# Kernel optimization log

Measured on AMD Instinct MI355X. Metric: run time of the kernel, lower is better.

Reference implementation:

```python
import jax, jax.numpy as jnp
import numpy as np

# dims: NL layers, D=d_model, DI=expand*D, F=d_ff, V=vocab, L=S*C seq, R=dt_rank, N=d_state, K=d_conv
NL, D, DI, F, V, L, R, N, K = 2, 256, 512, 1024, 1024, 1024, 16, 16, 4
B, S, C = 2, 128, 8
EPS = 1e-5


def silu(x):
    return x * jax.nn.sigmoid(x)


def batchnorm(x, g, b):  # x: [B,L,D], normalize over (B,L) per channel (training-mode BatchNorm1d)
    m = x.mean((0, 1))
    v = x.var((0, 1))
    return (x - m) * jax.lax.rsqrt(v + EPS) * g + b


def layernorm(x, g, b):
    m = x.mean(-1, keepdims=True)
    v = x.var(-1, keepdims=True)
    return (x - m) * jax.lax.rsqrt(v + EPS) * g + b


def mamba(x, Win, cw, cb, Wx, Wdt, bdt, A_log, Dsk, Wout, bout):
    # x: [B,L,D] -> [B,L,D]; standard Mamba block with selective scan
    Bsz, Lseq, _ = x.shape
    xz = x @ Win                      # [B,L,2*DI]
    xi, z = jnp.split(xz, 2, axis=-1)
    # depthwise causal conv1d, width K
    xp = jnp.pad(xi, ((0, 0), (K - 1, 0), (0, 0)))
    xc = cb + sum(xp[:, k:k + Lseq, :] * cw[:, k] for k in range(K))
    xc = silu(xc)                     # [B,L,DI]
    xdb = xc @ Wx                     # [B,L,R+2N]
    delta = jax.nn.softplus(xdb[..., :R] @ Wdt + bdt)   # [B,L,DI]
    Bm = xdb[..., R:R + N]            # [B,L,N]
    Cm = xdb[..., R + N:]             # [B,L,N]
    A = -jnp.exp(A_log)               # [DI,N]
    dA = jnp.exp(delta[..., None] * A)                       # [B,L,DI,N]
    dBx = delta[..., None] * Bm[:, :, None, :] * xc[..., None]  # [B,L,DI,N]

    def step(h, inp):
        dA_t, dBx_t, C_t = inp
        h = h * dA_t + dBx_t          # [B,DI,N]
        y = jnp.einsum('bdn,bn->bd', h, C_t)
        return h, y

    h0 = jnp.zeros((Bsz, DI, N), x.dtype)
    _, ys = jax.lax.scan(step, h0, (dA.transpose(1, 0, 2, 3), dBx.transpose(1, 0, 2, 3), Cm.transpose(1, 0, 2)))
    y = ys.transpose(1, 0, 2) + Dsk * xc
    y = y * silu(z)
    return y @ Wout + bout


def _forward(input_ids, emb, pos, Win, conv_w, conv_b, Wx, Wdt, bdt, A_log, Dskip, Wout, bout,
             bn_g, bn_b, ln_g, ln_b, ff_w1, ff_b1, ff_w2, ff_b2, final_w, final_b):
    Bsz, Ssz, Csz = input_ids.shape
    Lseq = Ssz * Csz
    # Encoder: token embedding (scaled) + learned positions, flattened to [B, S*C, D]
    x = emb[input_ids].reshape(Bsz, Lseq, D) * jnp.sqrt(jnp.float32(D)) + pos[:Lseq]
    for i in range(NL):
        f = mamba(x, Win[i, 0], conv_w[i, 0], conv_b[i, 0], Wx[i, 0], Wdt[i, 0], bdt[i, 0],
                  A_log[i, 0], Dskip[i, 0], Wout[i, 0], bout[i, 0])
        f = batchnorm(f, bn_g[i, 0], bn_b[i, 0])
        bk = mamba(x[:, ::-1], Win[i, 1], conv_w[i, 1], conv_b[i, 1], Wx[i, 1], Wdt[i, 1], bdt[i, 1],
                   A_log[i, 1], Dskip[i, 1], Wout[i, 1], bout[i, 1])
        bk = batchnorm(bk, bn_g[i, 1], bn_b[i, 1])[:, ::-1]
        f = layernorm(x + f, ln_g[i, 0], ln_b[i, 0])
        bk = layernorm(x + bk, ln_g[i, 1], ln_b[i, 1])
        out = f + bk
        out = jax.nn.relu(out @ ff_w1[i] + ff_b1[i]) @ ff_w2[i] + ff_b2[i]
        out = batchnorm(out, bn_g[i, 2], bn_b[i, 2])
        x = out + x
    return x.reshape(Bsz, Ssz, Csz, D) @ final_w + final_b   # [B,S,C,V]


def setup_inputs() -> dict:
    key = jax.random.key(0)
    ks = list(jax.random.split(key, 16))
    kit = iter(ks)
    rn = lambda shape, s=0.02: jax.random.normal(next(kit), shape, jnp.float32) * s
    inp = {
        'input_ids': jax.random.randint(next(kit), (B, S, C), 0, V),
        'emb': rn((V, D)), 'pos': rn((L, D)),
        'Win': rn((NL, 2, D, 2 * DI)),
        'conv_w': rn((NL, 2, DI, K), 0.1), 'conv_b': jnp.zeros((NL, 2, DI)),
        'Wx': rn((NL, 2, DI, R + 2 * N)),
        'Wdt': rn((NL, 2, R, DI)), 'bdt': jnp.full((NL, 2, DI), -4.0),
        'A_log': jnp.broadcast_to(jnp.log(jnp.arange(1, N + 1, dtype=jnp.float32)), (NL, 2, DI, N)) + 0.0,
        'Dskip': jnp.ones((NL, 2, DI)),
        'Wout': rn((NL, 2, DI, D)), 'bout': jnp.zeros((NL, 2, D)),
        'bn_g': jnp.ones((NL, 3, D)), 'bn_b': jnp.zeros((NL, 3, D)),
        'ln_g': jnp.ones((NL, 2, D)), 'ln_b': jnp.zeros((NL, 2, D)),
        'ff_w1': rn((NL, D, F)), 'ff_b1': jnp.zeros((NL, F)),
        'ff_w2': rn((NL, F, D)), 'ff_b2': jnp.zeros((NL, D)),
        'final_w': rn((D, V)), 'final_b': jnp.zeros((V,)),
    }
    return inp


def reference(input_ids, emb, pos, Win, conv_w, conv_b, Wx, Wdt, bdt, A_log, Dskip, Wout, bout,
              bn_g, bn_b, ln_g, ln_b, ff_w1, ff_b1, ff_w2, ff_b2, final_w, final_b):
    return _forward(input_ids, emb, pos, Win, conv_w, conv_b, Wx, Wdt, bdt, A_log, Dskip, Wout, bout,
                    bn_g, bn_b, ln_g, ln_b, ff_w1, ff_b1, ff_w2, ff_b2, final_w, final_b)
```

## Files before the change

kernel.cpp:

```cpp
#include <hip/hip_runtime.h>

#define NL 2
#define DMODEL 256
#define DI 512
#define FF 1024
#define VV 1024
#define LSEQ 1024
#define RR 16
#define NN 16
#define KCONV 4
#define BTOK 2048
#define EPS 1e-5f

using short8 = __attribute__((ext_vector_type(8))) short;
using float4v = __attribute__((ext_vector_type(4))) float;
typedef unsigned short u16;

__device__ inline float bf2f(u16 u) {
    union { unsigned u; float f; } x; x.u = (unsigned)u << 16; return x.f;
}
__device__ inline u16 f2bf(float f) {
    union { float f; unsigned u; } x; x.f = f;
    unsigned r = x.u + 0x7fffu + ((x.u >> 16) & 1u);
    return (u16)(r >> 16);
}

#if __has_builtin(__builtin_amdgcn_exp2f)
#define EXP2(x) __builtin_amdgcn_exp2f(x)
#else
#define EXP2(x) exp2f(x)
#endif

struct TMat { const float* src; u16* dst; int rows, cols, tile0, tilecols; };
struct TTable { TMat m[24]; int nmat; };

__global__ __launch_bounds__(256) void transpose_kernel(TTable tt) {
    __shared__ u16 tile[32][33];
    int bx = blockIdx.x;
    int j = 0;
    for (int k = 1; k < tt.nmat; ++k) if (bx >= tt.m[k].tile0) j = k;
    TMat mm = tt.m[j];
    int lt = bx - mm.tile0;
    int r0 = (lt / mm.tilecols) * 32, c0 = (lt % mm.tilecols) * 32;
    int tx = threadIdx.x & 31, ty = threadIdx.x >> 5;
    #pragma unroll
    for (int k = 0; k < 4; ++k) {
        int r = r0 + ty + k * 8, c = c0 + tx;
        tile[ty + k * 8][tx] = (r < mm.rows && c < mm.cols) ? f2bf(mm.src[(size_t)r * mm.cols + c]) : (u16)0;
    }
    __syncthreads();
    #pragma unroll
    for (int k = 0; k < 4; ++k) {
        int c = c0 + ty + k * 8, r = r0 + tx;
        if (c < mm.cols && r < mm.rows) mm.dst[(size_t)c * mm.rows + r] = tile[tx][ty + k * 8];
    }
}

template<int BN, int WR, int WC, int RT, int CT>
__global__ __launch_bounds__(256) void sgemm_kernel(
    const u16* __restrict__ A0, int lda, unsigned long long sA,
    const u16* __restrict__ B0, int ldb, unsigned long long sB,
    const float* __restrict__ bias0, unsigned long long sBias,
    void* __restrict__ C0, int ldc, unsigned long long sC,
    int K, int act, int outfp)
{
    constexpr int BM = 128, BK = 32;
    __shared__ u16 As[BM * BK];
    __shared__ u16 Bs[BN * BK];
    const u16* A = A0 + (size_t)blockIdx.z * sA;
    const u16* Bt = B0 + (size_t)blockIdx.z * sB;
    const float* bias = bias0 ? (bias0 + (size_t)blockIdx.z * sBias) : nullptr;

    const int tid = threadIdx.x, w = tid >> 6, lane = tid & 63;
    const int row0 = blockIdx.y * BM, col0 = blockIdx.x * BN;
    const int wr = w / WC, wc = w % WC;
    const int mi = lane & 15, kq = lane >> 4;
    const int lr = lane >> 2, lc = (lane & 3) * 8;

    float4v acc[RT][CT];
    #pragma unroll
    for (int i = 0; i < RT; ++i)
        #pragma unroll
        for (int j = 0; j < CT; ++j) acc[i][j] = (float4v){0.f, 0.f, 0.f, 0.f};

    for (int kk = 0; kk < K; kk += BK) {
        __syncthreads();
        for (int i = w; i < BM / 16; i += 4) {
            const u16* g = A + (size_t)(row0 + i * 16 + lr) * lda + kk + lc;
            __builtin_amdgcn_global_load_lds(
                (const __attribute__((address_space(1))) void*)g,
                (__attribute__((address_space(3))) void*)(As + i * 16 * BK), 16, 0, 0);
        }
        for (int i = w; i < BN / 16; i += 4) {
            const u16* g = Bt + (size_t)(col0 + i * 16 + lr) * ldb + kk + lc;
            __builtin_amdgcn_global_load_lds(
                (const __attribute__((address_space(1))) void*)g,
                (__attribute__((address_space(3))) void*)(Bs + i * 16 * BK), 16, 0, 0);
        }
        __syncthreads();
        short8 af[RT], bf[CT];
        #pragma unroll
        for (int i = 0; i < RT; ++i)
            af[i] = *(const short8*)(As + (wr * RT * 16 + i * 16 + mi) * BK + kq * 8);
        #pragma unroll
        for (int j = 0; j < CT; ++j)
            bf[j] = *(const short8*)(Bs + (wc * CT * 16 + j * 16 + mi) * BK + kq * 8);
        #pragma unroll
        for (int i = 0; i < RT; ++i)
            #pragma unroll
            for (int j = 0; j < CT; ++j)
                acc[i][j] = __builtin_amdgcn_mfma_f32_16x16x32_bf16(af[i], bf[j], acc[i][j], 0, 0, 0);
    }

    #pragma unroll
    for (int i = 0; i < RT; ++i)
        #pragma unroll
        for (int j = 0; j < CT; ++j) {
            int n = col0 + wc * CT * 16 + j * 16 + mi;
            float bv = bias ? bias[n] : 0.f;
            #pragma unroll
            for (int r = 0; r < 4; ++r) {
                int m = row0 + wr * RT * 16 + i * 16 + kq * 4 + r;
                float v = acc[i][j][r] + bv;
                if (act == 1) v = fmaxf(v, 0.f);
                if (outfp)
                    ((float*)C0)[(size_t)blockIdx.z * sC + (size_t)m * ldc + n] = v;
                else
                    ((u16*)C0)[(size_t)blockIdx.z * sC + (size_t)m * ldc + n] = f2bf(v);
            }
        }
}

__global__ __launch_bounds__(256) void gemm_kernel(
    const u16* __restrict__ A0, int lda, unsigned long long sA,
    const u16* __restrict__ B0, int ldb, unsigned long long sB,
    const float* __restrict__ bias0, unsigned long long sBias,
    void* __restrict__ C0, int ldc, unsigned long long sC,
    int M, int N, int K, int act, int outfp)
{
    const u16* A = A0 + (size_t)blockIdx.z * sA;
    const u16* Bt = B0 + (size_t)blockIdx.z * sB;
    const float* bias = bias0 ? (bias0 + (size_t)blockIdx.z * sBias) : nullptr;

    int tid = threadIdx.x;
    int wv = tid >> 6, lane = tid & 63;
    int row0 = blockIdx.y * 64 + (wv >> 1) * 32;
    int col0 = blockIdx.x * 64 + (wv & 1) * 32;
    int mi = lane & 15, kq = lane >> 4;

    float4v acc[2][2];
    #pragma unroll
    for (int a = 0; a < 2; ++a)
        #pragma unroll
        for (int b = 0; b < 2; ++b) acc[a][b] = (float4v){0.f, 0.f, 0.f, 0.f};
    const short8 zer = {0, 0, 0, 0, 0, 0, 0, 0};

    for (int kk = 0; kk < K; kk += 32) {
        int k = kk + kq * 8;
        bool kv = (k < K);
        short8 af[2], bf[2];
        #pragma unroll
        for (int rt = 0; rt < 2; ++rt) {
            int r = row0 + rt * 16 + mi;
            af[rt] = kv ? *(const short8*)(A + (size_t)r * lda + k) : zer;
        }
        #pragma unroll
        for (int ct = 0; ct < 2; ++ct) {
            int n = col0 + ct * 16 + mi;
            bf[ct] = (kv && n < N) ? *(const short8*)(Bt + (size_t)n * ldb + k) : zer;
        }
        #pragma unroll
        for (int rt = 0; rt < 2; ++rt)
            #pragma unroll
            for (int ct = 0; ct < 2; ++ct)
                acc[rt][ct] = __builtin_amdgcn_mfma_f32_16x16x32_bf16(af[rt], bf[ct], acc[rt][ct], 0, 0, 0);
    }

    #pragma unroll
    for (int rt = 0; rt < 2; ++rt)
        #pragma unroll
        for (int ct = 0; ct < 2; ++ct) {
            int n = col0 + ct * 16 + mi;
            if (n >= N) continue;
            float bv = bias ? bias[n] : 0.f;
            #pragma unroll
            for (int r = 0; r < 4; ++r) {
                int m = row0 + rt * 16 + kq * 4 + r;
                float v = acc[rt][ct][r] + bv;
                if (act == 1) v = fmaxf(v, 0.f);
                if (outfp)
                    ((float*)C0)[(size_t)blockIdx.z * sC + (size_t)m * ldc + n] = v;
                else
                    ((u16*)C0)[(size_t)blockIdx.z * sC + (size_t)m * ldc + n] = f2bf(v);
            }
        }
}

__global__ __launch_bounds__(256) void delta_fused_kernel(
    const u16* __restrict__ xdb, const u16* __restrict__ wdtT,
    const float* __restrict__ bdt, const u16* __restrict__ xc,
    u16* __restrict__ deltaT, u16* __restrict__ uT, int layer)
{
    int z = blockIdx.z;
    const u16* A = xdb + (size_t)z * BTOK * 48;
    const u16* Bt = wdtT + (size_t)z * 512 * 16;
    const float* bias = bdt + (size_t)z * 512;

    int tid = threadIdx.x;
    int wv = tid >> 6, lane = tid & 63;
    int row0 = blockIdx.y * 64 + (wv >> 1) * 32;
    int col0 = blockIdx.x * 64 + (wv & 1) * 32;
    int mi = lane & 15, kq = lane >> 4;

    float4v acc[2][2];
    #pragma unroll
    for (int a = 0; a < 2; ++a)
        #pragma unroll
        for (int b = 0; b < 2; ++b) acc[a][b] = (float4v){0.f, 0.f, 0.f, 0.f};
    const short8 zer = {0, 0, 0, 0, 0, 0, 0, 0};

    int k = kq * 8;
    bool kv = (k < 16);
    short8 af[2], bf[2];
    #pragma unroll
    for (int rt = 0; rt < 2; ++rt) {
        int r = row0 + rt * 16 + mi;
        af[rt] = kv ? *(const short8*)(A + (size_t)r * 48 + k) : zer;
    }
    #pragma unroll
    for (int ct = 0; ct < 2; ++ct) {
        int n = col0 + ct * 16 + mi;
        bf[ct] = kv ? *(const short8*)(Bt + (size_t)n * 16 + k) : zer;
    }
    #pragma unroll
    for (int rt = 0; rt < 2; ++rt)
        #pragma unroll
        for (int ct = 0; ct < 2; ++ct)
            acc[rt][ct] = __builtin_amdgcn_mfma_f32_16x16x32_bf16(af[rt], bf[ct], acc[rt][ct], 0, 0, 0);

    #pragma unroll
    for (int rt = 0; rt < 2; ++rt)
        #pragma unroll
        for (int ct = 0; ct < 2; ++ct) {
            int n = col0 + ct * 16 + mi;
            float bv = bias[n];
            #pragma unroll
            for (int r = 0; r < 4; ++r) {
                int m = row0 + rt * 16 + kq * 4 + r;
                float v = acc[rt][ct][r] + bv;
                v = (v > 20.f) ? v : logf(1.f + __expf(v));
                float xcv = bf2f(xc[((size_t)z * BTOK + m) * DI + n]);
                int b = m >> 10, t = m & 1023;
                size_t off = ((size_t)((z * 2 + b) * DI + n)) * LSEQ + t;
                deltaT[off] = f2bf(v);
                uT[off] = f2bf(v * xcv);
            }
        }
}

__global__ __launch_bounds__(256) void bct_kernel(
    const u16* __restrict__ xdb, u16* __restrict__ bcT)
{
    __shared__ u16 tile[32][34];
    int slab = blockIdx.y;
    int t0 = blockIdx.x * 32;
    int tx = threadIdx.x & 31, ty = threadIdx.x >> 5;
    #pragma unroll
    for (int k = 0; k < 4; ++k) {
        int t = t0 + ty + k * 8;
        tile[tx][ty + k * 8] = xdb[(size_t)(slab * 1024 + t) * 48 + 16 + tx];
    }
    __syncthreads();
    #pragma unroll
    for (int k = 0; k < 4; ++k) {
        int col = ty + k * 8;
        bcT[((size_t)(slab * 32 + col)) * LSEQ + t0 + tx] = tile[col][tx];
    }
}

__global__ __launch_bounds__(256) void embed_kernel(
    const int* __restrict__ ids, const float* __restrict__ emb,
    const float* __restrict__ pos, u16* __restrict__ x)
{
    int tok = blockIdx.x, d = threadIdx.x;
    int id = ids[tok];
    float v = emb[(size_t)id * DMODEL + d] * 16.0f + pos[(size_t)(tok & (LSEQ - 1)) * DMODEL + d];
    x[(size_t)tok * DMODEL + d] = f2bf(v);
}

__global__ __launch_bounds__(256) void conv_kernel(
    const u16* __restrict__ xz, const float* __restrict__ conv_w,
    const float* __restrict__ conv_b, u16* __restrict__ xc, int layer)
{
    unsigned g = blockIdx.x * 256u + threadIdx.x;
    int d = g & 511;
    int t = (g >> 9) & 1023;
    int b = (g >> 19) & 1;
    int dir = g >> 20;
    int wbase = ((layer * 2 + dir) * DI + d);
    float acc = conv_b[wbase];
    int colbase = dir * 1024 + d;
    #pragma unroll
    for (int k = 0; k < KCONV; ++k) {
        int ts = dir ? (t + 3 - k) : (t - 3 + k);
        if (ts >= 0 && ts < LSEQ)
            acc += conv_w[wbase * KCONV + k] * bf2f(xz[(size_t)((b << 10) + ts) * 2048 + colbase]);
    }
    float v = acc / (1.f + __expf(-acc));
    xc[(size_t)(((dir * 2 + b) << 10) + t) * DI + d] = f2bf(v);
}

template<int DIR>
__device__ __forceinline__ void scan_body(
    const u16* __restrict__ deltaT, const u16* __restrict__ uT,
    const u16* __restrict__ bcT, const float* __restrict__ A_log,
    u16* __restrict__ pT, int layer, int slab,
    float* Ps, float* Qs)
{
    const int c = threadIdx.x;
    const int d = blockIdx.x;

    float a2[16];
    const float* al = A_log + (size_t)(((layer * 2 + DIR) * DI + d) * NN);
    #pragma unroll
    for (int n = 0; n < 16; ++n) a2[n] = -__expf(al[n]) * 1.44269504f;

    const size_t tb = ((size_t)(slab * DI + d)) * LSEQ;
    const size_t bcb = (size_t)slab * 32 * LSEQ;
    const int T0 = DIR ? (1016 - 8 * c) : (8 * c);

    short8 dlv = *(const short8*)(deltaT + tb + T0);
    short8 uvv = *(const short8*)(uT + tb + T0);
    float dls[8], uvs[8];
    #pragma unroll
    for (int s = 0; s < 8; ++s) {
        const int idx = DIR ? 7 - s : s;
        dls[s] = bf2f((u16)dlv[idx]);
        uvs[s] = bf2f((u16)uvv[idx]);
    }

    const int base = c * 17;
    #pragma unroll
    for (int n = 0; n < 16; ++n) {
        short8 B8 = *(const short8*)(bcT + bcb + (size_t)n * LSEQ + T0);
        float P = 1.f, Q = 0.f;
        #pragma unroll
        for (int s = 0; s < 8; ++s) {
            const int idx = DIR ? 7 - s : s;
            float dA = EXP2(dls[s] * a2[n]);
            Q = Q * dA + uvs[s] * bf2f((u16)B8[idx]);
            P *= dA;
        }
        Ps[base + n] = P;
        Qs[base + n] = Q;
    }
    __syncthreads();

    for (int off = 1; off < 128; off <<= 1) {
        float np[16], nq[16];
        const bool act = (c >= off);
        if (act) {
            const int nb = (c - off) * 17;
            #pragma unroll
            for (int n = 0; n < 16; ++n) { np[n] = Ps[nb + n]; nq[n] = Qs[nb + n]; }
        }
        __syncthreads();
        if (act) {
            #pragma unroll
            for (int n = 0; n < 16; ++n) {
                float p = Ps[base + n], q = Qs[base + n];
                Qs[base + n] = fmaf(p, nq[n], q);
                Ps[base + n] = p * np[n];
            }
        }
        __syncthreads();
    }

    float pacc[8];
    #pragma unroll
    for (int s = 0; s < 8; ++s) pacc[s] = 0.f;
    const int hb = (c - 1) * 17;
    #pragma unroll
    for (int n = 0; n < 16; ++n) {
        short8 B8 = *(const short8*)(bcT + bcb + (size_t)n * LSEQ + T0);
        short8 C8 = *(const short8*)(bcT + bcb + (size_t)(16 + n) * LSEQ + T0);
        float h = (c == 0) ? 0.f : Qs[hb + n];
        #pragma unroll
        for (int s = 0; s < 8; ++s) {
            const int idx = DIR ? 7 - s : s;
            float dA = EXP2(dls[s] * a2[n]);
            h = h * dA + uvs[s] * bf2f((u16)B8[idx]);
            pacc[s] = fmaf(h, bf2f((u16)C8[idx]), pacc[s]);
        }
    }
    short8 pk;
    #pragma unroll
    for (int s = 0; s < 8; ++s) {
        const int idx = DIR ? 7 - s : s;
        pk[idx] = (short)f2bf(pacc[s]);
    }
    *(short8*)(pT + tb + T0) = pk;
}

__global__ __launch_bounds__(128) void scan_kernel(
    const u16* __restrict__ deltaT, const u16* __restrict__ uT,
    const u16* __restrict__ bcT, const float* __restrict__ A_log,
    u16* __restrict__ pT, int layer)
{
    __shared__ float Ps[128 * 17], Qs[128 * 17];
    int slab = blockIdx.y;
    if (slab >> 1)
        scan_body<1>(deltaT, uT, bcT, A_log, pT, layer, slab, Ps, Qs);
    else
        scan_body<0>(deltaT, uT, bcT, A_log, pT, layer, slab, Ps, Qs);
}

__global__ __launch_bounds__(256) void gate_kernel(
    const u16* __restrict__ pT, const u16* __restrict__ xc,
    const u16* __restrict__ xz, const float* __restrict__ Dskip,
    u16* __restrict__ y, int layer)
{
    __shared__ float tile[32][33];
    int z = blockIdx.z, dir = z >> 1, b = z & 1;
    int d0 = blockIdx.x * 32, t0 = blockIdx.y * 32;
    int tx = threadIdx.x & 31, ty = threadIdx.x >> 5;
    #pragma unroll
    for (int k = 0; k < 4; ++k) {
        int d = d0 + ty + k * 8;
        tile[ty + k * 8][tx] = bf2f(pT[((size_t)(z * DI + d)) * LSEQ + t0 + tx]);
    }
    __syncthreads();
    #pragma unroll
    for (int k = 0; k < 4; ++k) {
        int t = t0 + ty + k * 8, d = d0 + tx;
        float p = tile[tx][ty + k * 8];
        float xcv = bf2f(xc[(size_t)((z << 10) + t) * DI + d]);
        float zv = bf2f(xz[(size_t)((b << 10) + t) * 2048 + dir * 1024 + 512 + d]);
        float dsk = Dskip[(layer * 2 + dir) * DI + d];
        float yv = (p + dsk * xcv) * (zv / (1.f + __expf(-zv)));
        y[(size_t)((z << 10) + t) * DI + d] = f2bf(yv);
    }
}

__global__ __launch_bounds__(256) void bnstats_kernel(
    const u16* __restrict__ p0, const u16* __restrict__ p1, float* __restrict__ stats)
{
    int d = blockIdx.x, arr = blockIdx.y, tid = threadIdx.x;
    const u16* p = arr ? p1 : p0;
    float s = 0.f, q = 0.f;
    #pragma unroll
    for (int k = 0; k < 8; ++k) {
        float v = bf2f(p[(size_t)(tid + k * 256) * DMODEL + d]);
        s += v; q += v * v;
    }
    #pragma unroll
    for (int off = 1; off < 64; off <<= 1) { s += __shfl_xor(s, off); q += __shfl_xor(q, off); }
    __shared__ float ss[4], qs[4];
    if ((tid & 63) == 0) { ss[tid >> 6] = s; qs[tid >> 6] = q; }
    __syncthreads();
    if (tid == 0) {
        float S = ss[0] + ss[1] + ss[2] + ss[3];
        float Q2 = qs[0] + qs[1] + qs[2] + qs[3];
        float mean = S * (1.f / 2048.f);
        float var = Q2 * (1.f / 2048.f) - mean * mean;
        stats[(arr * DMODEL + d) * 2] = mean;
        stats[(arr * DMODEL + d) * 2 + 1] = rsqrtf(var + EPS);
    }
}

__global__ __launch_bounds__(256) void fuseln_kernel(
    const u16* __restrict__ x, const u16* __restrict__ outm, const float* __restrict__ stats,
    const float* __restrict__ bng, const float* __restrict__ bnb,
    const float* __restrict__ lng, const float* __restrict__ lnb, u16* __restrict__ ffin)
{
    int tok = blockIdx.x, d = threadIdx.x;
    float xv = bf2f(x[(size_t)tok * DMODEL + d]);
    float of = bf2f(outm[(size_t)tok * DMODEL + d]);
    float ob = bf2f(outm[(size_t)BTOK * DMODEL + (size_t)tok * DMODEL + d]);
    float vf = xv + (of - stats[d * 2]) * stats[d * 2 + 1] * bng[d] + bnb[d];
    float vb = xv + (ob - stats[(DMODEL + d) * 2]) * stats[(DMODEL + d) * 2 + 1] * bng[DMODEL + d] + bnb[DMODEL + d];
    float s0 = vf, s1 = vf * vf, s2 = vb, s3 = vb * vb;
    #pragma unroll
    for (int off = 1; off < 64; off <<= 1) {
        s0 += __shfl_xor(s0, off); s1 += __shfl_xor(s1, off);
        s2 += __shfl_xor(s2, off); s3 += __shfl_xor(s3, off);
    }
    __shared__ float sm[4][4];
    if ((d & 63) == 0) { sm[d >> 6][0] = s0; sm[d >> 6][1] = s1; sm[d >> 6][2] = s2; sm[d >> 6][3] = s3; }
    __syncthreads();
    s0 = sm[0][0] + sm[1][0] + sm[2][0] + sm[3][0];
    s1 = sm[0][1] + sm[1][1] + sm[2][1] + sm[3][1];
    s2 = sm[0][2] + sm[1][2] + sm[2][2] + sm[3][2];
    s3 = sm[0][3] + sm[1][3] + sm[2][3] + sm[3][3];
    float mf = s0 * (1.f / 256.f), vvf = s1 * (1.f / 256.f) - mf * mf;
    float mb = s2 * (1.f / 256.f), vvb = s3 * (1.f / 256.f) - mb * mb;
    float fl = (vf - mf) * rsqrtf(vvf + EPS) * lng[d] + lnb[d];
    float bl = (vb - mb) * rsqrtf(vvb + EPS) * lng[DMODEL + d] + lnb[DMODEL + d];
    ffin[(size_t)tok * DMODEL + d] = f2bf(fl + bl);
}

__global__ __launch_bounds__(256) void bnadd_kernel(
    u16* __restrict__ x, const u16* __restrict__ ffo, const float* __restrict__ stats,
    const float* __restrict__ g, const float* __restrict__ b)
{
    int tok = blockIdx.x, d = threadIdx.x;
    size_t idx = (size_t)tok * DMODEL + d;
    float v = bf2f(x[idx]) + (bf2f(ffo[idx]) - stats[d * 2]) * stats[d * 2 + 1] * g[d] + b[d];
    x[idx] = f2bf(v);
}

extern "C" void kernel_launch(void* const* d_in, const int* in_sizes, int n_in,
                              void* d_out, int out_size, void* d_ws, size_t ws_size,
                              hipStream_t stream)
{
    const int*   ids     = (const int*)d_in[0];
    const float* emb     = (const float*)d_in[1];
    const float* pos     = (const float*)d_in[2];
    const float* Win     = (const float*)d_in[3];
    const float* conv_w  = (const float*)d_in[4];
    const float* conv_b  = (const float*)d_in[5];
    const float* Wx      = (const float*)d_in[6];
    const float* Wdt     = (const float*)d_in[7];
    const float* bdt     = (const float*)d_in[8];
    const float* A_log   = (const float*)d_in[9];
    const float* Dskip   = (const float*)d_in[10];
    const float* Wout    = (const float*)d_in[11];
    const float* bout    = (const float*)d_in[12];
    const float* bn_g    = (const float*)d_in[13];
    const float* bn_b    = (const float*)d_in[14];
    const float* ln_g    = (const float*)d_in[15];
    const float* ln_b    = (const float*)d_in[16];
    const float* ff_w1   = (const float*)d_in[17];
    const float* ff_b1   = (const float*)d_in[18];
    const float* ff_w2   = (const float*)d_in[19];
    const float* ff_b2   = (const float*)d_in[20];
    const float* final_w = (const float*)d_in[21];
    const float* final_b = (const float*)d_in[22];

    char* cur = (char*)d_ws;
    auto alloc = [&](size_t elems) {
        u16* p = (u16*)cur;
        cur += ((elems * 2 + 511) / 512) * 512;
        return p;
    };
    u16* winT  = alloc((size_t)NL * 2048 * 256);
    u16* wxT   = alloc((size_t)NL * 2 * 48 * 512);
    u16* wdtT  = alloc((size_t)NL * 2 * 512 * 16);
    u16* woutT = alloc((size_t)NL * 2 * 256 * 512);
    u16* fw1T  = alloc((size_t)NL * 1024 * 256);
    u16* fw2T  = alloc((size_t)NL * 256 * 1024);
    u16* finT  = alloc((size_t)1024 * 256);
    u16* xbuf   = alloc((size_t)BTOK * DMODEL);
    u16* xz     = alloc((size_t)BTOK * 2048);
    u16* xc     = alloc((size_t)2 * BTOK * DI);
    u16* xdb    = alloc((size_t)2 * BTOK * 48);
    u16* bcT    = alloc((size_t)4 * 32 * LSEQ);
    u16* deltaT = alloc((size_t)2 * BTOK * DI);
    u16* uT     = alloc((size_t)2 * BTOK * DI);
    u16* pT     = alloc((size_t)2 * BTOK * DI);
    u16* ybuf   = alloc((size_t)2 * BTOK * DI);
    u16* outm   = alloc((size_t)2 * BTOK * DMODEL);
    u16* ffin   = alloc((size_t)BTOK * DMODEL);
    u16* ffh    = alloc((size_t)BTOK * FF);
    u16* ffo    = alloc((size_t)BTOK * DMODEL);
    float* statsM = (float*)alloc(4096);
    float* statsF = statsM + 1024;

    TTable tt; int nm = 0, tiles = 0;
    auto addT = [&](const float* src, u16* dst, int rows, int cols) {
        int tc = (cols + 31) / 32, tr = (rows + 31) / 32;
        tt.m[nm] = {src, dst, rows, cols, tiles, tc};
        tiles += tc * tr; nm++;
    };
    for (int i = 0; i < NL; ++i) {
        for (int dir = 0; dir < 2; ++dir) {
            addT(Win  + (size_t)(i * 2 + dir) * 256 * 1024, winT  + (size_t)i * 2048 * 256 + (size_t)dir * 1024 * 256, 256, 1024);
            addT(Wx   + (size_t)(i * 2 + dir) * 512 * 48,   wxT   + (size_t)(i * 2 + dir) * 48 * 512,   512, 48);
            addT(Wdt  + (size_t)(i * 2 + dir) * 16 * 512,   wdtT  + (size_t)(i * 2 + dir) * 512 * 16,   16, 512);
            addT(Wout + (size_t)(i * 2 + dir) * 512 * 256,  woutT + (size_t)(i * 2 + dir) * 256 * 512,  512, 256);
        }
        addT(ff_w1 + (size_t)i * 256 * 1024, fw1T + (size_t)i * 1024 * 256, 256, 1024);
        addT(ff_w2 + (size_t)i * 1024 * 256, fw2T + (size_t)i * 256 * 1024, 1024, 256);
    }
    addT(final_w, finT, 256, 1024);
    tt.nmat = nm;
    transpose_kernel<<<tiles, 256, 0, stream>>>(tt);

    embed_kernel<<<BTOK, 256, 0, stream>>>(ids, emb, pos, xbuf);

    auto gemm = [&](const u16* A, int lda, size_t sA, const u16* Bt, int ldb, size_t sB,
                    const float* bias, size_t sBias, void* C, int ldc, size_t sC,
                    int M, int N, int K, int act, int nb, int outfp) {
        dim3 g((N + 63) / 64, M / 64, nb);
        gemm_kernel<<<g, 256, 0, stream>>>(A, lda, (unsigned long long)sA, Bt, ldb, (unsigned long long)sB,
                                           bias, (unsigned long long)sBias, C, ldc, (unsigned long long)sC,
                                           M, N, K, act, outfp);
    };
    auto sgemm128 = [&](const u16* A, int lda, const u16* Bt, int ldb, size_t sB,
                        const float* bias, size_t sBias, void* C, int ldc,
                        int N, int K, int act, int nb, int outfp) {
        dim3 g(N / 128, BTOK / 128, nb);
        sgemm_kernel<128, 2, 2, 4, 4><<<g, 256, 0, stream>>>(
            A, lda, 0ULL, Bt, ldb, (unsigned long long)sB, bias, (unsigned long long)sBias,
            C, ldc, 0ULL, K, act, outfp);
    };
    auto sgemm64 = [&](const u16* A, int lda, size_t sA, const u16* Bt, int ldb, size_t sB,
                       const float* bias, size_t sBias, void* C, int ldc, size_t sC,
                       int N, int K, int act, int nb, int outfp) {
        dim3 g(N / 64, BTOK / 128, nb);
        sgemm_kernel<64, 4, 1, 2, 4><<<g, 256, 0, stream>>>(
            A, lda, (unsigned long long)sA, Bt, ldb, (unsigned long long)sB,
            bias, (unsigned long long)sBias, C, ldc, (unsigned long long)sC, K, act, outfp);
    };

    for (int i = 0; i < NL; ++i) {
        sgemm128(xbuf, 256, winT + (size_t)i * 2048 * 256, 256, 0, nullptr, 0,
                 xz, 2048, 2048, 256, 0, 1, 0);
        conv_kernel<<<(2 * BTOK * DI) / 256, 256, 0, stream>>>(xz, conv_w, conv_b, xc, i);
        gemm(xc, 512, (size_t)BTOK * 512, wxT + (size_t)i * 2 * 48 * 512, 512, 48 * 512,
             nullptr, 0, xdb, 48, (size_t)BTOK * 48, BTOK, 48, 512, 0, 2, 0);
        bct_kernel<<<dim3(32, 4), 256, 0, stream>>>(xdb, bcT);
        delta_fused_kernel<<<dim3(8, 32, 2), 256, 0, stream>>>(
            xdb, wdtT + (size_t)i * 2 * 512 * 16, bdt + (size_t)i * 2 * 512, xc, deltaT, uT, i);
        scan_kernel<<<dim3(512, 4), 128, 0, stream>>>(deltaT, uT, bcT, A_log, pT, i);
        gate_kernel<<<dim3(DI / 32, LSEQ / 32, 4), 256, 0, stream>>>(pT, xc, xz, Dskip, ybuf, i);
        sgemm64(ybuf, 512, (size_t)BTOK * 512, woutT + (size_t)i * 2 * 256 * 512, 512, 256 * 512,
                bout + (size_t)i * 2 * 256, 256, outm, 256, (size_t)BTOK * 256, 256, 512, 0, 2, 0);
        bnstats_kernel<<<dim3(256, 2), 256, 0, stream>>>(outm, outm + (size_t)BTOK * 256, statsM);
        fuseln_kernel<<<BTOK, 256, 0, stream>>>(xbuf, outm, statsM,
            bn_g + (size_t)i * 3 * 256, bn_b + (size_t)i * 3 * 256,
            ln_g + (size_t)i * 2 * 256, ln_b + (size_t)i * 2 * 256, ffin);
        sgemm128(ffin, 256, fw1T + (size_t)i * 1024 * 256, 256, 0,
                 ff_b1 + (size_t)i * 1024, 0, ffh, 1024, 1024, 256, 1, 1, 0);
        sgemm64(ffh, 1024, 0, fw2T + (size_t)i * 256 * 1024, 1024, 0,
                ff_b2 + (size_t)i * 256, 0, ffo, 256, 0, 256, 1024, 0, 1, 0);
        bnstats_kernel<<<dim3(256, 1), 256, 0, stream>>>(ffo, ffo, statsF);
        bnadd_kernel<<<BTOK, 256, 0, stream>>>(xbuf, ffo, statsF,
            bn_g + (size_t)(i * 3 + 2) * 256, bn_b + (size_t)(i * 3 + 2) * 256);
    }
    sgemm128(xbuf, 256, finT, 256, 0, final_b, 0,
             d_out, 1024, 1024, 256, 0, 1, 1);
}
```

Measured before the change: 434.8 us.

## Fuse BatchNorm statistics and B/C transpose into GEMM epilogues, retune GEMM tiles

The standalone bnstats kernels are removed. Each output GEMM epilogue now accumulates per-column sum and sum of squares via wave shuffles and float atomics into stats buffers, which are zeroed by earlier kernels (gate, fuseln). The separate bct transpose kernel is folded into the xdb GEMM epilogue as strided transposed stores. GEMM tile shapes change so more blocks launch for the small-N matmuls. This saves launches and re-reads of outm/ffo and xdb, at the cost of atomic contention, scattered stores and E[x²]-mean² variance with reordered float sums.

```diff
diff --git a/kernel.cpp b/kernel.cpp
--- a/kernel.cpp
+++ b/kernel.cpp
@@ -56,15 +56,15 @@
     }
 }
 
-template<int BN, int WR, int WC, int RT, int CT>
+template<int BM, int BN, int WR, int WC, int RT, int CT>
 __global__ __launch_bounds__(256) void sgemm_kernel(
     const u16* __restrict__ A0, int lda, unsigned long long sA,
     const u16* __restrict__ B0, int ldb, unsigned long long sB,
     const float* __restrict__ bias0, unsigned long long sBias,
     void* __restrict__ C0, int ldc, unsigned long long sC,
-    int K, int act, int outfp)
-{
-    constexpr int BM = 128, BK = 32;
+    int K, int act, int outfp, float* __restrict__ stats, int statsStride)
+{
+    constexpr int BK = 32;
     __shared__ u16 As[BM * BK];
     __shared__ u16 Bs[BN * BK];
     const u16* A = A0 + (size_t)blockIdx.z * sA;
@@ -113,11 +113,12 @@
     }
 
     #pragma unroll
-    for (int i = 0; i < RT; ++i)
-        #pragma unroll
-        for (int j = 0; j < CT; ++j) {
-            int n = col0 + wc * CT * 16 + j * 16 + mi;
-            float bv = bias ? bias[n] : 0.f;
+    for (int j = 0; j < CT; ++j) {
+        const int n = col0 + wc * CT * 16 + j * 16 + mi;
+        const float bv = bias ? bias[n] : 0.f;
+        float s = 0.f, q = 0.f;
+        #pragma unroll
+        for (int i = 0; i < RT; ++i) {
             #pragma unroll
             for (int r = 0; r < 4; ++r) {
                 int m = row0 + wr * RT * 16 + i * 16 + kq * 4 + r;
@@ -127,8 +128,18 @@
                     ((float*)C0)[(size_t)blockIdx.z * sC + (size_t)m * ldc + n] = v;
                 else
                     ((u16*)C0)[(size_t)blockIdx.z * sC + (size_t)m * ldc + n] = f2bf(v);
+                s += v; q += v * v;
             }
         }
+        if (stats) {
+            s += __shfl_xor(s, 16); s += __shfl_xor(s, 32);
+            q += __shfl_xor(q, 16); q += __shfl_xor(q, 32);
+            if (lane < 16) {
+                atomicAdd(&stats[(size_t)(blockIdx.z * statsStride + n) * 2], s);
+                atomicAdd(&stats[(size_t)(blockIdx.z * statsStride + n) * 2 + 1], q);
+            }
+        }
+    }
 }
 
 __global__ __launch_bounds__(256) void gemm_kernel(
@@ -136,7 +147,7 @@
     const u16* __restrict__ B0, int ldb, unsigned long long sB,
     const float* __restrict__ bias0, unsigned long long sBias,
     void* __restrict__ C0, int ldc, unsigned long long sC,
-    int M, int N, int K, int act, int outfp)
+    int M, int N, int K, int act, int outfp, u16* __restrict__ bcT0)
 {
     const u16* A = A0 + (size_t)blockIdx.z * sA;
     const u16* Bt = B0 + (size_t)blockIdx.z * sB;
@@ -188,10 +199,15 @@
                 int m = row0 + rt * 16 + kq * 4 + r;
                 float v = acc[rt][ct][r] + bv;
                 if (act == 1) v = fmaxf(v, 0.f);
+                u16 hv = f2bf(v);
                 if (outfp)
                     ((float*)C0)[(size_t)blockIdx.z * sC + (size_t)m * ldc + n] = v;
                 else
-                    ((u16*)C0)[(size_t)blockIdx.z * sC + (size_t)m * ldc + n] = f2bf(v);
+                    ((u16*)C0)[(size_t)blockIdx.z * sC + (size_t)m * ldc + n] = hv;
+                if (bcT0 && n >= 16) {
+                    int bb = m >> 10, t = m & 1023;
+                    bcT0[((size_t)((blockIdx.z * 2 + bb) * 32 + (n - 16))) * LSEQ + t] = hv;
+                }
             }
         }
 }
@@ -258,26 +274,6 @@
         }
 }
 
-__global__ __launch_bounds__(256) void bct_kernel(
-    const u16* __restrict__ xdb, u16* __restrict__ bcT)
-{
-    __shared__ u16 tile[32][34];
-    int slab = blockIdx.y;
-    int t0 = blockIdx.x * 32;
-    int tx = threadIdx.x & 31, ty = threadIdx.x >> 5;
-    #pragma unroll
-    for (int k = 0; k < 4; ++k) {
-        int t = t0 + ty + k * 8;
-        tile[tx][ty + k * 8] = xdb[(size_t)(slab * 1024 + t) * 48 + 16 + tx];
-    }
-    __syncthreads();
-    #pragma unroll
-    for (int k = 0; k < 4; ++k) {
-        int col = ty + k * 8;
-        bcT[((size_t)(slab * 32 + col)) * LSEQ + t0 + tx] = tile[col][tx];
-    }
-}
-
 __global__ __launch_bounds__(256) void embed_kernel(
     const int* __restrict__ ids, const float* __restrict__ emb,
     const float* __restrict__ pos, u16* __restrict__ x)
@@ -418,8 +414,11 @@
 __global__ __launch_bounds__(256) void gate_kernel(
     const u16* __restrict__ pT, const u16* __restrict__ xc,
     const u16* __restrict__ xz, const float* __restrict__ Dskip,
-    u16* __restrict__ y, int layer)
-{
+    u16* __restrict__ y, float* __restrict__ statsM, int layer)
+{
+    if (blockIdx.x == 0 && blockIdx.y == 0 && blockIdx.z == 0) {
+        for (int k = threadIdx.x; k < 2048; k += 256) statsM[k] = 0.f;
+    }
     __shared__ float tile[32][33];
     int z = blockIdx.z, dir = z >> 1, b = z & 1;
     int d0 = blockIdx.x * 32, t0 = blockIdx.y * 32;
@@ -442,43 +441,23 @@
     }
 }
 
-__global__ __launch_bounds__(256) void bnstats_kernel(
-    const u16* __restrict__ p0, const u16* __restrict__ p1, float* __restrict__ stats)
-{
-    int d = blockIdx.x, arr = blockIdx.y, tid = threadIdx.x;
-    const u16* p = arr ? p1 : p0;
-    float s = 0.f, q = 0.f;
-    #pragma unroll
-    for (int k = 0; k < 8; ++k) {
-        float v = bf2f(p[(size_t)(tid + k * 256) * DMODEL + d]);
-        s += v; q += v * v;
-    }
-    #pragma unroll
-    for (int off = 1; off < 64; off <<= 1) { s += __shfl_xor(s, off); q += __shfl_xor(q, off); }
-    __shared__ float ss[4], qs[4];
-    if ((tid & 63) == 0) { ss[tid >> 6] = s; qs[tid >> 6] = q; }
-    __syncthreads();
-    if (tid == 0) {
-        float S = ss[0] + ss[1] + ss[2] + ss[3];
-        float Q2 = qs[0] + qs[1] + qs[2] + qs[3];
-        float mean = S * (1.f / 2048.f);
-        float var = Q2 * (1.f / 2048.f) - mean * mean;
-        stats[(arr * DMODEL + d) * 2] = mean;
-        stats[(arr * DMODEL + d) * 2 + 1] = rsqrtf(var + EPS);
-    }
-}
-
 __global__ __launch_bounds__(256) void fuseln_kernel(
     const u16* __restrict__ x, const u16* __restrict__ outm, const float* __restrict__ stats,
     const float* __restrict__ bng, const float* __restrict__ bnb,
-    const float* __restrict__ lng, const float* __restrict__ lnb, u16* __restrict__ ffin)
+    const float* __restrict__ lng, const float* __restrict__ lnb,
+    u16* __restrict__ ffin, float* __restrict__ statsF)
 {
     int tok = blockIdx.x, d = threadIdx.x;
+    if (tok == 0) { for (int k = d; k < 512; k += 256) statsF[k] = 0.f; }
     float xv = bf2f(x[(size_t)tok * DMODEL + d]);
     float of = bf2f(outm[(size_t)tok * DMODEL + d]);
     float ob = bf2f(outm[(size_t)BTOK * DMODEL + (size_t)tok * DMODEL + d]);
-    float vf = xv + (of - stats[d * 2]) * stats[d * 2 + 1] * bng[d] + bnb[d];
-    float vb = xv + (ob - stats[(DMODEL + d) * 2]) * stats[(DMODEL + d) * 2 + 1] * bng[DMODEL + d] + bnb[DMODEL + d];
+    float mf0 = stats[d * 2] * (1.f / 2048.f);
+    float rf0 = rsqrtf(stats[d * 2 + 1] * (1.f / 2048.f) - mf0 * mf0 + EPS);
+    float mb0 = stats[(DMODEL + d) * 2] * (1.f / 2048.f);
+    float rb0 = rsqrtf(stats[(DMODEL + d) * 2 + 1] * (1.f / 2048.f) - mb0 * mb0 + EPS);
+    float vf = xv + (of - mf0) * rf0 * bng[d] + bnb[d];
+    float vb = xv + (ob - mb0) * rb0 * bng[DMODEL + d] + bnb[DMODEL + d];
     float s0 = vf, s1 = vf * vf, s2 = vb, s3 = vb * vb;
     #pragma unroll
     for (int off = 1; off < 64; off <<= 1) {
@@ -505,7 +484,9 @@
 {
     int tok = blockIdx.x, d = threadIdx.x;
     size_t idx = (size_t)tok * DMODEL + d;
-    float v = bf2f(x[idx]) + (bf2f(ffo[idx]) - stats[d * 2]) * stats[d * 2 + 1] * g[d] + b[d];
+    float mean = stats[d * 2] * (1.f / 2048.f);
+    float rs = rsqrtf(stats[d * 2 + 1] * (1.f / 2048.f) - mean * mean + EPS);
+    float v = bf2f(x[idx]) + (bf2f(ffo[idx]) - mean) * rs * g[d] + b[d];
     x[idx] = f2bf(v);
 }
 
@@ -564,7 +545,7 @@
     u16* ffh    = alloc((size_t)BTOK * FF);
     u16* ffo    = alloc((size_t)BTOK * DMODEL);
     float* statsM = (float*)alloc(4096);
-    float* statsF = statsM + 1024;
+    float* statsF = statsM + 2048;
 
     TTable tt; int nm = 0, tiles = 0;
     auto addT = [&](const float* src, u16* dst, int rows, int cols) {
@@ -588,56 +569,37 @@
 
     embed_kernel<<<BTOK, 256, 0, stream>>>(ids, emb, pos, xbuf);
 
-    auto gemm = [&](const u16* A, int lda, size_t sA, const u16* Bt, int ldb, size_t sB,
-                    const float* bias, size_t sBias, void* C, int ldc, size_t sC,
-                    int M, int N, int K, int act, int nb, int outfp) {
-        dim3 g((N + 63) / 64, M / 64, nb);
-        gemm_kernel<<<g, 256, 0, stream>>>(A, lda, (unsigned long long)sA, Bt, ldb, (unsigned long long)sB,
-                                           bias, (unsigned long long)sBias, C, ldc, (unsigned long long)sC,
-                                           M, N, K, act, outfp);
-    };
-    auto sgemm128 = [&](const u16* A, int lda, const u16* Bt, int ldb, size_t sB,
-                        const float* bias, size_t sBias, void* C, int ldc,
-                        int N, int K, int act, int nb, int outfp) {
-        dim3 g(N / 128, BTOK / 128, nb);
-        sgemm_kernel<128, 2, 2, 4, 4><<<g, 256, 0, stream>>>(
-            A, lda, 0ULL, Bt, ldb, (unsigned long long)sB, bias, (unsigned long long)sBias,
-            C, ldc, 0ULL, K, act, outfp);
-    };
-    auto sgemm64 = [&](const u16* A, int lda, size_t sA, const u16* Bt, int ldb, size_t sB,
-                       const float* bias, size_t sBias, void* C, int ldc, size_t sC,
-                       int N, int K, int act, int nb, int outfp) {
-        dim3 g(N / 64, BTOK / 128, nb);
-        sgemm_kernel<64, 4, 1, 2, 4><<<g, 256, 0, stream>>>(
-            A, lda, (unsigned long long)sA, Bt, ldb, (unsigned long long)sB,
-            bias, (unsigned long long)sBias, C, ldc, (unsigned long long)sC, K, act, outfp);
-    };
-
     for (int i = 0; i < NL; ++i) {
-        sgemm128(xbuf, 256, winT + (size_t)i * 2048 * 256, 256, 0, nullptr, 0,
-                 xz, 2048, 2048, 256, 0, 1, 0);
+        sgemm_kernel<128, 128, 2, 2, 4, 4><<<dim3(16, 16), 256, 0, stream>>>(
+            xbuf, 256, 0ULL, winT + (size_t)i * 2048 * 256, 256, 0ULL, nullptr, 0ULL,
+            xz, 2048, 0ULL, 256, 0, 0, nullptr, 0);
         conv_kernel<<<(2 * BTOK * DI) / 256, 256, 0, stream>>>(xz, conv_w, conv_b, xc, i);
-        gemm(xc, 512, (size_t)BTOK * 512, wxT + (size_t)i * 2 * 48 * 512, 512, 48 * 512,
-             nullptr, 0, xdb, 48, (size_t)BTOK * 48, BTOK, 48, 512, 0, 2, 0);
-        bct_kernel<<<dim3(32, 4), 256, 0, stream>>>(xdb, bcT);
+        gemm_kernel<<<dim3(1, 32, 2), 256, 0, stream>>>(
+            xc, 512, (unsigned long long)((size_t)BTOK * 512),
+            wxT + (size_t)i * 2 * 48 * 512, 512, 48ULL * 512, nullptr, 0ULL,
+            xdb, 48, (unsigned long long)((size_t)BTOK * 48), BTOK, 48, 512, 0, 0, bcT);
         delta_fused_kernel<<<dim3(8, 32, 2), 256, 0, stream>>>(
             xdb, wdtT + (size_t)i * 2 * 512 * 16, bdt + (size_t)i * 2 * 512, xc, deltaT, uT, i);
         scan_kernel<<<dim3(512, 4), 128, 0, stream>>>(deltaT, uT, bcT, A_log, pT, i);
-        gate_kernel<<<dim3(DI / 32, LSEQ / 32, 4), 256, 0, stream>>>(pT, xc, xz, Dskip, ybuf, i);
-        sgemm64(ybuf, 512, (size_t)BTOK * 512, woutT + (size_t)i * 2 * 256 * 512, 512, 256 * 512,
-                bout + (size_t)i * 2 * 256, 256, outm, 256, (size_t)BTOK * 256, 256, 512, 0, 2, 0);
-        bnstats_kernel<<<dim3(256, 2), 256, 0, stream>>>(outm, outm + (size_t)BTOK * 256, statsM);
+        gate_kernel<<<dim3(DI / 32, LSEQ / 32, 4), 256, 0, stream>>>(pT, xc, xz, Dskip, ybuf, statsM, i);
+        sgemm_kernel<64, 64, 2, 2, 2, 2><<<dim3(4, 32, 2), 256, 0, stream>>>(
+            ybuf, 512, (unsigned long long)((size_t)BTOK * 512),
+            woutT + (size_t)i * 2 * 256 * 512, 512, 256ULL * 512,
+            bout + (size_t)i * 2 * 256, 256ULL,
+            outm, 256, (unsigned long long)((size_t)BTOK * 256), 512, 0, 0, statsM, 256);
         fuseln_kernel<<<BTOK, 256, 0, stream>>>(xbuf, outm, statsM,
             bn_g + (size_t)i * 3 * 256, bn_b + (size_t)i * 3 * 256,
-            ln_g + (size_t)i * 2 * 256, ln_b + (size_t)i * 2 * 256, ffin);
-        sgemm128(ffin, 256, fw1T + (size_t)i * 1024 * 256, 256, 0,
-                 ff_b1 + (size_t)i * 1024, 0, ffh, 1024, 1024, 256, 1, 1, 0);
-        sgemm64(ffh, 1024, 0, fw2T + (size_t)i * 256 * 1024, 1024, 0,
-                ff_b2 + (size_t)i * 256, 0, ffo, 256, 0, 256, 1024, 0, 1, 0);
-        bnstats_kernel<<<dim3(256, 1), 256, 0, stream>>>(ffo, ffo, statsF);
+            ln_g + (size_t)i * 2 * 256, ln_b + (size_t)i * 2 * 256, ffin, statsF);
+        sgemm_kernel<128, 64, 4, 1, 2, 4><<<dim3(16, 16), 256, 0, stream>>>(
+            ffin, 256, 0ULL, fw1T + (size_t)i * 1024 * 256, 256, 0ULL,
+            ff_b1 + (size_t)i * 1024, 0ULL, ffh, 1024, 0ULL, 256, 1, 0, nullptr, 0);
+        sgemm_kernel<64, 64, 2, 2, 2, 2><<<dim3(4, 32), 256, 0, stream>>>(
+            ffh, 1024, 0ULL, fw2T + (size_t)i * 256 * 1024, 1024, 0ULL,
+            ff_b2 + (size_t)i * 256, 0ULL, ffo, 256, 0ULL, 1024, 0, 0, statsF, 0);
         bnadd_kernel<<<BTOK, 256, 0, stream>>>(xbuf, ffo, statsF,
             bn_g + (size_t)(i * 3 + 2) * 256, bn_b + (size_t)(i * 3 + 2) * 256);
     }
-    sgemm128(xbuf, 256, finT, 256, 0, final_b, 0,
-             d_out, 1024, 1024, 256, 0, 1, 1);
-}
+    sgemm_kernel<128, 64, 4, 1, 2, 4><<<dim3(16, 16), 256, 0, stream>>>(
+        xbuf, 256, 0ULL, finT, 256, 0ULL, final_b, 0ULL,
+        d_out, 1024, 0ULL, 256, 0, 1, nullptr, 0);
+}
```

New measurement: 387.8 us. 10.8% less time.
